# Kernel optimization log

Measured on AMD Instinct MI355X. Metric: run time of the kernel, lower is better.

## Reference

```python
import jax, jax.numpy as jnp
import numpy as np

T, B, H, L = 512, 64, 512, 2  # seq_len, batch, hidden(=input), num_layers


def setup_inputs() -> dict:
    key = jax.random.key(0)
    ks = jax.random.split(key, 15)
    s = 1.0 / np.sqrt(H)
    u = lambda k, shape: jax.random.uniform(k, shape, jnp.float32, -s, s)
    return {
        "sequence_r": jax.random.normal(ks[0], (T, B, H), jnp.float32),
        "sequence_i": jax.random.normal(ks[1], (T, B, H), jnp.float32),
        "h0_r": jax.random.normal(ks[2], (L, B, H), jnp.float32),
        "h0_i": jax.random.normal(ks[3], (L, B, H), jnp.float32),
        "c0_r": jax.random.normal(ks[4], (L, B, H), jnp.float32),
        "c0_i": jax.random.normal(ks[5], (L, B, H), jnp.float32),
        # complexLinear weights: real and imag parts of input->4H and hidden->4H maps
        "Wi_r": u(ks[6], (L, 4 * H, H)),
        "Wi_i": u(ks[7], (L, 4 * H, H)),
        "Wh_r": u(ks[8], (L, 4 * H, H)),
        "Wh_i": u(ks[9], (L, 4 * H, H)),
        "bi_r": u(ks[10], (L, 4 * H)),
        "bi_i": u(ks[11], (L, 4 * H)),
        "bh_r": u(ks[12], (L, 4 * H)),
        "bh_i": u(ks[13], (L, 4 * H)),
    }


def _run_layer(xr, xi, hr, hi, cr, ci, wir, wii, whr, whi, bir, bii, bhr, bhi):
    # Precompute the input projection for all timesteps (complex matmul): [T,B,4H]
    pr = jnp.einsum('tbd,gd->tbg', xr, wir) - jnp.einsum('tbd,gd->tbg', xi, wii) + bir
    pi = jnp.einsum('tbd,gd->tbg', xi, wir) + jnp.einsum('tbd,gd->tbg', xr, wii) + bii

    def step(carry, p):
        hr, hi, cr, ci = carry
        prt, pit = p
        # complex hidden projection
        gr = prt + hr @ whr.T - hi @ whi.T + bhr  # [B,4H]
        gi = pit + hi @ whr.T + hr @ whi.T + bhi
        ir_, fr_, gr_, or_ = jnp.split(gr, 4, axis=-1)
        ii_, fi_, gi_, oi_ = jnp.split(gi, 4, axis=-1)
        # split-type complex activations: act(real) + 1j*act(imag)
        i_r, i_i = jax.nn.sigmoid(ir_), jax.nn.sigmoid(ii_)
        f_r, f_i = jax.nn.sigmoid(fr_), jax.nn.sigmoid(fi_)
        o_r, o_i = jax.nn.sigmoid(or_), jax.nn.sigmoid(oi_)
        g_r, g_i = jnp.tanh(gr_), jnp.tanh(gi_)
        # c = f*c + i*g  (complex multiply)
        cr2 = f_r * cr - f_i * ci + i_r * g_r - i_i * g_i
        ci2 = f_r * ci + f_i * cr + i_r * g_i + i_i * g_r
        # h = o * tanh(c)
        t_r, t_i = jnp.tanh(cr2), jnp.tanh(ci2)
        hr2 = o_r * t_r - o_i * t_i
        hi2 = o_r * t_i + o_i * t_r
        return (hr2, hi2, cr2, ci2), (hr2, hi2)

    (hr, hi, cr, ci), (yr, yi) = jax.lax.scan(step, (hr, hi, cr, ci), (pr, pi))
    return yr, yi, hr, hi


def reference(sequence_r, sequence_i, h0_r, h0_i, c0_r, c0_i,
              Wi_r, Wi_i, Wh_r, Wh_i, bi_r, bi_i, bh_r, bh_i):
    xr, xi = sequence_r, sequence_i
    fin_r, fin_i = [], []
    for l in range(h0_r.shape[0]):
        xr, xi, hr, hi = _run_layer(
            xr, xi, h0_r[l], h0_i[l], c0_r[l], c0_i[l],
            Wi_r[l], Wi_i[l], Wh_r[l], Wh_i[l],
            bi_r[l], bi_i[l], bh_r[l], bh_i[l])
        fin_r.append(hr)
        fin_i.append(hi)
    return xr, xi, jnp.stack(fin_r), jnp.stack(fin_i)
```

## Files before the change

### kernel.cpp

```cpp
#include <hip/hip_runtime.h>
#include <stdint.h>


#define NPHASE 514

typedef __attribute__((ext_vector_type(8))) short short8;
typedef __attribute__((ext_vector_type(4))) float floatx4;
typedef float __attribute__((ext_vector_type(4))) floatv4;
typedef __attribute__((ext_vector_type(4))) unsigned int uintx4;

#define OFF_W    32768u
#define SZ_W     (2u*4096u*2048u*2u)
#define OFF_BIAS (OFF_W + SZ_W)
#define SZ_BIAS  (2u*4096u*4u)
#define OFF_H    (OFF_BIAS + SZ_BIAS)
#define SZ_H     (2u*4u*64u*512u*4u)
#define OFF_XBF  (OFF_H + SZ_H)
#define SZ_XBF   (512u*64u*1024u*2u)
#define NEED_XBF ((size_t)OFF_XBF + SZ_XBF)

__device__ __forceinline__ unsigned short f2bf(float f) {
  union { float f; uint32_t u; } v; v.f = f;
  uint32_t u = v.u;
  uint32_t r = (u + 0x7fffu + ((u >> 16) & 1u)) >> 16;
  return (unsigned short)r;
}
__device__ __forceinline__ float sigm(float x)  { return 1.0f / (1.0f + __expf(-x)); }
__device__ __forceinline__ float tanhf_(float x){ return 1.0f - 2.0f / (1.0f + __expf(2.0f * x)); }

__device__ __forceinline__ uintx4 ld_bypass_b128(const uint32_t* p) {
  uintx4 r;
  asm volatile("global_load_dwordx4 %0, %1, off sc0 sc1" : "=v"(r) : "v"(p));
  return r;
}
__device__ __forceinline__ void wait_vm0() {
  asm volatile("s_waitcnt vmcnt(0)" ::: "memory");
  __builtin_amdgcn_sched_barrier(0);
}


__global__ void pack_weights_k(const float* __restrict__ Wi_r, const float* __restrict__ Wi_i,
                               const float* __restrict__ Wh_r, const float* __restrict__ Wh_i,
                               unsigned short* __restrict__ wp) {
  uint32_t idx = blockIdx.x * 256u + threadIdx.x;
  int j    = idx & 7;
  int lane = (idx >> 3) & 63;
  int nt   = (idx >> 9) & 1;
  int kt   = (idx >> 10) & 63;
  int nb   = (idx >> 16) & 127;
  int l    = idx >> 23;
  int mrow = lane & 15, quad = lane >> 4;
  int n_col = nt * 16 + mrow;
  int dd = n_col >> 3, g = n_col & 7;
  int jrow = (g & 3) * 512 + nb * 4 + dd;
  int k = kt * 32 + quad * 8 + j;
  bool im = (g >= 4);
  size_t ro = ((size_t)l * 2048 + jrow) * 512;
  float v;
  if (k < 1024 && l == 0) {
    int seg = k >> 9, kk = k & 511;
    if (seg == 0) v = im ? Wi_i[ro + kk] :  Wi_r[ro + kk];
    else          v = im ? Wi_r[ro + kk] : -Wi_i[ro + kk];
  } else {
    int kk = k & 1023;
    int d = kk >> 1, ri = kk & 1;
    const float* Wr = (k < 1024) ? Wi_r : Wh_r;
    const float* Wm = (k < 1024) ? Wi_i : Wh_i;
    if (ri == 0) v = im ? Wm[ro + d] :  Wr[ro + d];
    else         v = im ? Wr[ro + d] : -Wm[ro + d];
  }
  wp[idx] = f2bf(v);
}

__global__ void pack_bias_k(const float* __restrict__ bi_r, const float* __restrict__ bi_i,
                            const float* __restrict__ bh_r, const float* __restrict__ bh_i,
                            float* __restrict__ bp) {
  uint32_t idx = blockIdx.x * 256u + threadIdx.x;
  int n_col = idx & 31, nb = (idx >> 5) & 127, l = idx >> 12;
  int dd = n_col >> 3, g = n_col & 7;
  int j = (g & 3) * 512 + nb * 4 + dd;
  float v = (g >= 4) ? (bi_i[l * 2048 + j] + bh_i[l * 2048 + j])
                     : (bi_r[l * 2048 + j] + bh_r[l * 2048 + j]);
  bp[idx] = v;
}

__global__ void init_state_k(const float* __restrict__ h0_r, const float* __restrict__ h0_i,
                             uint32_t* __restrict__ hring32, uint32_t* __restrict__ bar) {
  uint32_t idx = blockIdx.x * 256u + threadIdx.x;
  if (idx < 8192) bar[idx] = 0;
  int d = idx & 511, b = (idx >> 9) & 63, l = idx >> 15;
  int slot = (2 * l + 3) & 3;
  uint32_t* row = hring32 + (((size_t)l * 4 + slot) * 64 + b) * 512;
  row[d] = ((uint32_t)f2bf(h0_i[idx]) << 16) | (uint32_t)f2bf(h0_r[idx]);
}

__global__ void convert_x_k(const float* __restrict__ xr, const float* __restrict__ xi,
                            unsigned short* __restrict__ xbf) {
  uint32_t idx = blockIdx.x * 256u + threadIdx.x;
  int k = idx & 1023;
  uint32_t row = idx >> 10;
  float v = (k < 512) ? xr[(size_t)row * 512 + k] : xi[(size_t)row * 512 + (k - 512)];
  xbf[idx] = f2bf(v);
}


__global__ __launch_bounds__(256, 1) void lstm_persist_k(
    const float* __restrict__ xr, const float* __restrict__ xi,
    const float* __restrict__ c0_r, const float* __restrict__ c0_i,
    const unsigned short* __restrict__ wp, const float* __restrict__ bp,
    uint32_t* __restrict__ hring32, const unsigned short* __restrict__ xbf,
    float* __restrict__ out, uint32_t* arr, uint32_t* gen_bc, int use_xbf)
{
  __shared__ short8 Wb[8192];
  __shared__ float Glds[64 * 33];
  __shared__ float bias_s[32];

  const int l   = blockIdx.x >> 7;
  const int nb  = blockIdx.x & 127;
  const int bid = blockIdx.x;
  const int tid = threadIdx.x;

  {
    const short8* src = (const short8*)(wp + (((size_t)l * 128 + nb) << 16));
    #pragma unroll
    for (int i = 0; i < 32; ++i) Wb[i * 256 + tid] = src[i * 256 + tid];
    if (tid < 32) bias_s[tid] = bp[(l * 128 + nb) * 32 + tid];
  }

  const int b_e = tid & 63, dd_e = tid >> 6;
  const int d_e = nb * 4 + dd_e;
  float cr = c0_r[(l * 64 + b_e) * 512 + d_e];
  float ci = c0_i[(l * 64 + b_e) * 512 + d_e];
  __syncthreads();

  const int wv = tid >> 6, lane = tid & 63;
  const int quad = lane >> 4, mrow = lane & 15;
  const int bm = wv * 16 + mrow;
  const bool cvt_path = (l == 0) && (!use_xbf);

  for (int p = 0; p < NPHASE; ++p) {
    const int t = p - 2 * l;
    const bool active = (t >= 0) && (t < 512);
    floatx4 acc0 = {0.f, 0.f, 0.f, 0.f}, acc1 = {0.f, 0.f, 0.f, 0.f};

    if (active) {
      if (l == 0) {
        if (cvt_path) {
          const size_t xtb = ((size_t)t * 64 + bm) * 512 + quad * 8;
          #pragma unroll 8
          for (int kt = 0; kt < 32; ++kt) {
            const float* xb = ((kt < 16) ? xr : xi) + xtb + (kt & 15) * 32;
            floatv4 f0 = *(const floatv4*)xb;
            floatv4 f1 = *(const floatv4*)(xb + 4);
            short8 a;
            #pragma unroll
            for (int jj = 0; jj < 4; ++jj) { a[jj] = (short)f2bf(f0[jj]); a[jj+4] = (short)f2bf(f1[jj]); }
            short8 bf0 = Wb[(kt * 2 + 0) * 64 + lane];
            short8 bf1 = Wb[(kt * 2 + 1) * 64 + lane];
            acc0 = __builtin_amdgcn_mfma_f32_16x16x32_bf16(a, bf0, acc0, 0, 0, 0);
            acc1 = __builtin_amdgcn_mfma_f32_16x16x32_bf16(a, bf1, acc1, 0, 0, 0);
          }
        } else {
          const unsigned short* xb = xbf + ((size_t)t * 64 + bm) * 1024 + quad * 8;
          #pragma unroll 8
          for (int kt = 0; kt < 32; ++kt) {
            short8 a = *(const short8*)(xb + kt * 32);
            short8 bf0 = Wb[(kt * 2 + 0) * 64 + lane];
            short8 bf1 = Wb[(kt * 2 + 1) * 64 + lane];
            acc0 = __builtin_amdgcn_mfma_f32_16x16x32_bf16(a, bf0, acc0, 0, 0, 0);
            acc1 = __builtin_amdgcn_mfma_f32_16x16x32_bf16(a, bf1, acc1, 0, 0, 0);
          }
        }
      } else {
        const uint32_t* xb = hring32 + (((size_t)0 * 4 + ((p - 2) & 3)) * 64 + bm) * 512 + quad * 4;
        uintx4 xp[32];
        #pragma unroll
        for (int i = 0; i < 32; ++i) xp[i] = ld_bypass_b128(xb + i * 16);
        wait_vm0();
        #pragma unroll
        for (int i = 0; i < 32; ++i) {
          short8 a = __builtin_bit_cast(short8, xp[i]);
          short8 bf0 = Wb[(i * 2 + 0) * 64 + lane];
          short8 bf1 = Wb[(i * 2 + 1) * 64 + lane];
          acc0 = __builtin_amdgcn_mfma_f32_16x16x32_bf16(a, bf0, acc0, 0, 0, 0);
          acc1 = __builtin_amdgcn_mfma_f32_16x16x32_bf16(a, bf1, acc1, 0, 0, 0);
        }
      }
    }

    {
      const uint32_t g = (uint32_t)p;
      long budget = (1L << 22);
      if (bid == 0) {
        if (tid > 0) {
          while (__hip_atomic_load(&arr[tid * 16], __ATOMIC_RELAXED, __HIP_MEMORY_SCOPE_AGENT) < g) {
            if (--budget <= 0) break;
          }
        }
        __syncthreads();
        __hip_atomic_store(&gen_bc[tid * 16], g, __ATOMIC_RELAXED, __HIP_MEMORY_SCOPE_AGENT);
      } else {
        if (tid < 64) {
          while (__hip_atomic_load(&gen_bc[bid * 16], __ATOMIC_RELAXED, __HIP_MEMORY_SCOPE_AGENT) < g) {
            if (--budget <= 0) break;
          }
        }
        __syncthreads();
      }
    }

    if (active) {
      const uint32_t* hb = hring32 + (((size_t)l * 4 + ((p - 1) & 3)) * 64 + bm) * 512 + quad * 4;
      uintx4 hp[32];
      #pragma unroll
      for (int i = 0; i < 32; ++i) hp[i] = ld_bypass_b128(hb + i * 16);
      wait_vm0();
      #pragma unroll
      for (int i = 0; i < 32; ++i) {
        short8 a = __builtin_bit_cast(short8, hp[i]);
        short8 bf0 = Wb[((32 + i) * 2 + 0) * 64 + lane];
        short8 bf1 = Wb[((32 + i) * 2 + 1) * 64 + lane];
        acc0 = __builtin_amdgcn_mfma_f32_16x16x32_bf16(a, bf0, acc0, 0, 0, 0);
        acc1 = __builtin_amdgcn_mfma_f32_16x16x32_bf16(a, bf1, acc1, 0, 0, 0);
      }
      const float bb0 = bias_s[mrow], bb1 = bias_s[16 + mrow];
      const int rowb = wv * 16 + quad * 4;
      #pragma unroll
      for (int r = 0; r < 4; ++r) {
        Glds[(rowb + r) * 33 + mrow]      = acc0[r] + bb0;
        Glds[(rowb + r) * 33 + 16 + mrow] = acc1[r] + bb1;
      }
    }
    __syncthreads();
    if (active) {
      const float* gp = &Glds[b_e * 33 + dd_e * 8];
      float i_r = sigm(gp[0]), f_r = sigm(gp[1]), gc_r = tanhf_(gp[2]), o_r = sigm(gp[3]);
      float i_i = sigm(gp[4]), f_i = sigm(gp[5]), gc_i = tanhf_(gp[6]), o_i = sigm(gp[7]);
      float cr2 = f_r * cr - f_i * ci + i_r * gc_r - i_i * gc_i;
      float ci2 = f_r * ci + f_i * cr + i_r * gc_i + i_i * gc_r;
      cr = cr2; ci = ci2;
      float t_r = tanhf_(cr), t_i = tanhf_(ci);
      float h_r = o_r * t_r - o_i * t_i;
      float h_i = o_r * t_i + o_i * t_r;
      uint32_t hpk = ((uint32_t)f2bf(h_i) << 16) | (uint32_t)f2bf(h_r);
      uint32_t* hw = hring32 + (((size_t)l * 4 + (p & 3)) * 64 + b_e) * 512;
      __hip_atomic_store(&hw[d_e], hpk, __ATOMIC_RELAXED, __HIP_MEMORY_SCOPE_AGENT);
      if (l == 1) {
        size_t o = ((size_t)t * 64 + b_e) * 512 + d_e;
        __hip_atomic_store((uint32_t*)(out + o), __float_as_uint(h_r),
                           __ATOMIC_RELAXED, __HIP_MEMORY_SCOPE_AGENT);
        __hip_atomic_store((uint32_t*)(out + 16777216 + o), __float_as_uint(h_i),
                           __ATOMIC_RELAXED, __HIP_MEMORY_SCOPE_AGENT);
      }
      if (t == 511) {
        size_t o = 33554432u + ((size_t)l * 64 + b_e) * 512 + d_e;
        __hip_atomic_store((uint32_t*)(out + o), __float_as_uint(h_r),
                           __ATOMIC_RELAXED, __HIP_MEMORY_SCOPE_AGENT);
        __hip_atomic_store((uint32_t*)(out + o + 65536), __float_as_uint(h_i),
                           __ATOMIC_RELAXED, __HIP_MEMORY_SCOPE_AGENT);
      }
    }
    __syncthreads();
    if (bid != 0 && tid == 0)
      __hip_atomic_store(&arr[bid * 16], (uint32_t)(p + 1),
                         __ATOMIC_RELAXED, __HIP_MEMORY_SCOPE_AGENT);
  }
}


extern "C" void kernel_launch(void* const* d_in, const int* in_sizes, int n_in,
                              void* d_out, int out_size, void* d_ws, size_t ws_size,
                              hipStream_t stream) {
  const float* seq_r = (const float*)d_in[0];
  const float* seq_i = (const float*)d_in[1];
  const float* h0_r  = (const float*)d_in[2];
  const float* h0_i  = (const float*)d_in[3];
  const float* c0_r  = (const float*)d_in[4];
  const float* c0_i  = (const float*)d_in[5];
  const float* Wi_r  = (const float*)d_in[6];
  const float* Wi_i  = (const float*)d_in[7];
  const float* Wh_r  = (const float*)d_in[8];
  const float* Wh_i  = (const float*)d_in[9];
  const float* bi_r  = (const float*)d_in[10];
  const float* bi_i  = (const float*)d_in[11];
  const float* bh_r  = (const float*)d_in[12];
  const float* bh_i  = (const float*)d_in[13];

  char* ws = (char*)d_ws;
  uint32_t* arr    = (uint32_t*)ws;
  uint32_t* gen_bc = (uint32_t*)(ws + 16384);
  unsigned short* wp   = (unsigned short*)(ws + OFF_W);
  float*          bias = (float*)(ws + OFF_BIAS);
  uint32_t*       hrg  = (uint32_t*)(ws + OFF_H);
  unsigned short* xbf  = (unsigned short*)(ws + OFF_XBF);
  const int use_xbf = (ws_size >= NEED_XBF) ? 1 : 0;

  pack_weights_k<<<65536, 256, 0, stream>>>(Wi_r, Wi_i, Wh_r, Wh_i, wp);
  pack_bias_k<<<32, 256, 0, stream>>>(bi_r, bi_i, bh_r, bh_i, bias);
  init_state_k<<<256, 256, 0, stream>>>(h0_r, h0_i, hrg, arr);
  if (use_xbf) convert_x_k<<<131072, 256, 0, stream>>>(seq_r, seq_i, xbf);

  lstm_persist_k<<<256, 256, 0, stream>>>(seq_r, seq_i, c0_r, c0_i, wp, bias,
                                          hrg, xbf, (float*)d_out, arr, gen_bc, use_xbf);
}
```

Before: 7.024 ms.

## Replace h ring buffer with full-history slots and coalesce h/output stores via LDS

Replaces the 4-slot hidden-state ring with a 513-slot history buffer per layer. Because each slot is written exactly once, readers can use ordinary cached loads with a pipelined unroll instead of cache-bypassing loads and a full vmcnt wait. It also stages each block's h values and outputs in LDS and writes them as 128-bit vector stores from single waves, rather than scalar atomic stores per thread. The history buffer needs much more workspace, and correctness now depends on cached loads never returning stale data for a slot written by another CU.

```diff
diff --git a/kernel.cpp b/kernel.cpp
--- a/kernel.cpp
+++ b/kernel.cpp
@@ -14,10 +14,11 @@
 #define OFF_BIAS (OFF_W + SZ_W)
 #define SZ_BIAS  (2u*4096u*4u)
 #define OFF_H    (OFF_BIAS + SZ_BIAS)
-#define SZ_H     (2u*4u*64u*512u*4u)
+#define SZ_H     (2u*513u*64u*512u*4u)
 #define OFF_XBF  (OFF_H + SZ_H)
 #define SZ_XBF   (512u*64u*1024u*2u)
-#define NEED_XBF ((size_t)OFF_XBF + SZ_XBF)
+#define NEED_HIST ((size_t)OFF_XBF)
+#define NEED_XBF  ((size_t)OFF_XBF + SZ_XBF)
 
 __device__ __forceinline__ unsigned short f2bf(float f) {
   union { float f; uint32_t u; } v; v.f = f;
@@ -32,6 +33,9 @@
   uintx4 r;
   asm volatile("global_load_dwordx4 %0, %1, off sc0 sc1" : "=v"(r) : "v"(p));
   return r;
+}
+__device__ __forceinline__ void st_thru_b128(uint32_t* p, uintx4 v) {
+  asm volatile("global_store_dwordx4 %0, %1, off sc0 sc1" :: "v"(p), "v"(v) : "memory");
 }
 __device__ __forceinline__ void wait_vm0() {
   asm volatile("s_waitcnt vmcnt(0)" ::: "memory");
@@ -85,12 +89,13 @@
 }
 
 __global__ void init_state_k(const float* __restrict__ h0_r, const float* __restrict__ h0_i,
-                             uint32_t* __restrict__ hring32, uint32_t* __restrict__ bar) {
+                             uint32_t* __restrict__ hist, uint32_t* __restrict__ bar,
+                             int use_hist) {
   uint32_t idx = blockIdx.x * 256u + threadIdx.x;
   if (idx < 8192) bar[idx] = 0;
   int d = idx & 511, b = (idx >> 9) & 63, l = idx >> 15;
-  int slot = (2 * l + 3) & 3;
-  uint32_t* row = hring32 + (((size_t)l * 4 + slot) * 64 + b) * 512;
+  size_t NS = use_hist ? 513 : 4;
+  uint32_t* row = hist + ((size_t)l * NS + 0) * 32768 + (size_t)b * 512;
   row[d] = ((uint32_t)f2bf(h0_i[idx]) << 16) | (uint32_t)f2bf(h0_r[idx]);
 }
 
@@ -108,12 +113,15 @@
     const float* __restrict__ xr, const float* __restrict__ xi,
     const float* __restrict__ c0_r, const float* __restrict__ c0_i,
     const unsigned short* __restrict__ wp, const float* __restrict__ bp,
-    uint32_t* __restrict__ hring32, const unsigned short* __restrict__ xbf,
-    float* __restrict__ out, uint32_t* arr, uint32_t* gen_bc, int use_xbf)
+    uint32_t* __restrict__ hist, const unsigned short* __restrict__ xbf,
+    float* __restrict__ out, uint32_t* arr, uint32_t* gen_bc,
+    int use_xbf, int use_hist)
 {
   __shared__ short8 Wb[8192];
   __shared__ float Glds[64 * 33];
   __shared__ float bias_s[32];
+  __shared__ uint32_t hbuf[64 * 4];
+  __shared__ float obr[64 * 4], obi[64 * 4];
 
   const int l   = blockIdx.x >> 7;
   const int nb  = blockIdx.x & 127;
@@ -137,6 +145,11 @@
   const int quad = lane >> 4, mrow = lane & 15;
   const int bm = wv * 16 + mrow;
   const bool cvt_path = (l == 0) && (!use_xbf);
+
+  const size_t NS = use_hist ? 513 : 4;
+  uint32_t* hbase_l = hist + (size_t)l * NS * 32768;
+  uint32_t* hbase_0 = hist;
+  auto sidx = [&](int s) -> size_t { return use_hist ? (size_t)s : (size_t)(s & 3); };
 
   for (int p = 0; p < NPHASE; ++p) {
     const int t = p - 2 * l;
@@ -172,18 +185,29 @@
           }
         }
       } else {
-        const uint32_t* xb = hring32 + (((size_t)0 * 4 + ((p - 2) & 3)) * 64 + bm) * 512 + quad * 4;
-        uintx4 xp[32];
-        #pragma unroll
-        for (int i = 0; i < 32; ++i) xp[i] = ld_bypass_b128(xb + i * 16);
-        wait_vm0();
-        #pragma unroll
-        for (int i = 0; i < 32; ++i) {
-          short8 a = __builtin_bit_cast(short8, xp[i]);
-          short8 bf0 = Wb[(i * 2 + 0) * 64 + lane];
-          short8 bf1 = Wb[(i * 2 + 1) * 64 + lane];
-          acc0 = __builtin_amdgcn_mfma_f32_16x16x32_bf16(a, bf0, acc0, 0, 0, 0);
-          acc1 = __builtin_amdgcn_mfma_f32_16x16x32_bf16(a, bf1, acc1, 0, 0, 0);
+        const uint32_t* xb = hbase_0 + sidx(p - 1) * 32768 + (size_t)bm * 512 + quad * 4;
+        if (use_hist) {
+          #pragma unroll 8
+          for (int i = 0; i < 32; ++i) {
+            short8 a = __builtin_bit_cast(short8, *(const uintx4*)(xb + i * 16));
+            short8 bf0 = Wb[(i * 2 + 0) * 64 + lane];
+            short8 bf1 = Wb[(i * 2 + 1) * 64 + lane];
+            acc0 = __builtin_amdgcn_mfma_f32_16x16x32_bf16(a, bf0, acc0, 0, 0, 0);
+            acc1 = __builtin_amdgcn_mfma_f32_16x16x32_bf16(a, bf1, acc1, 0, 0, 0);
+          }
+        } else {
+          uintx4 xp[32];
+          #pragma unroll
+          for (int i = 0; i < 32; ++i) xp[i] = ld_bypass_b128(xb + i * 16);
+          wait_vm0();
+          #pragma unroll
+          for (int i = 0; i < 32; ++i) {
+            short8 a = __builtin_bit_cast(short8, xp[i]);
+            short8 bf0 = Wb[(i * 2 + 0) * 64 + lane];
+            short8 bf1 = Wb[(i * 2 + 1) * 64 + lane];
+            acc0 = __builtin_amdgcn_mfma_f32_16x16x32_bf16(a, bf0, acc0, 0, 0, 0);
+            acc1 = __builtin_amdgcn_mfma_f32_16x16x32_bf16(a, bf1, acc1, 0, 0, 0);
+          }
         }
       }
     }
@@ -210,18 +234,29 @@
     }
 
     if (active) {
-      const uint32_t* hb = hring32 + (((size_t)l * 4 + ((p - 1) & 3)) * 64 + bm) * 512 + quad * 4;
-      uintx4 hp[32];
-      #pragma unroll
-      for (int i = 0; i < 32; ++i) hp[i] = ld_bypass_b128(hb + i * 16);
-      wait_vm0();
-      #pragma unroll
-      for (int i = 0; i < 32; ++i) {
-        short8 a = __builtin_bit_cast(short8, hp[i]);
-        short8 bf0 = Wb[((32 + i) * 2 + 0) * 64 + lane];
-        short8 bf1 = Wb[((32 + i) * 2 + 1) * 64 + lane];
-        acc0 = __builtin_amdgcn_mfma_f32_16x16x32_bf16(a, bf0, acc0, 0, 0, 0);
-        acc1 = __builtin_amdgcn_mfma_f32_16x16x32_bf16(a, bf1, acc1, 0, 0, 0);
+      const uint32_t* hb = hbase_l + sidx(t) * 32768 + (size_t)bm * 512 + quad * 4;
+      if (use_hist) {
+        #pragma unroll 8
+        for (int i = 0; i < 32; ++i) {
+          short8 a = __builtin_bit_cast(short8, *(const uintx4*)(hb + i * 16));
+          short8 bf0 = Wb[((32 + i) * 2 + 0) * 64 + lane];
+          short8 bf1 = Wb[((32 + i) * 2 + 1) * 64 + lane];
+          acc0 = __builtin_amdgcn_mfma_f32_16x16x32_bf16(a, bf0, acc0, 0, 0, 0);
+          acc1 = __builtin_amdgcn_mfma_f32_16x16x32_bf16(a, bf1, acc1, 0, 0, 0);
+        }
+      } else {
+        uintx4 hp[32];
+        #pragma unroll
+        for (int i = 0; i < 32; ++i) hp[i] = ld_bypass_b128(hb + i * 16);
+        wait_vm0();
+        #pragma unroll
+        for (int i = 0; i < 32; ++i) {
+          short8 a = __builtin_bit_cast(short8, hp[i]);
+          short8 bf0 = Wb[((32 + i) * 2 + 0) * 64 + lane];
+          short8 bf1 = Wb[((32 + i) * 2 + 1) * 64 + lane];
+          acc0 = __builtin_amdgcn_mfma_f32_16x16x32_bf16(a, bf0, acc0, 0, 0, 0);
+          acc1 = __builtin_amdgcn_mfma_f32_16x16x32_bf16(a, bf1, acc1, 0, 0, 0);
+        }
       }
       const float bb0 = bias_s[mrow], bb1 = bias_s[16 + mrow];
       const int rowb = wv * 16 + quad * 4;
@@ -232,6 +267,7 @@
       }
     }
     __syncthreads();
+
     if (active) {
       const float* gp = &Glds[b_e * 33 + dd_e * 8];
       float i_r = sigm(gp[0]), f_r = sigm(gp[1]), gc_r = tanhf_(gp[2]), o_r = sigm(gp[3]);
@@ -242,28 +278,35 @@
       float t_r = tanhf_(cr), t_i = tanhf_(ci);
       float h_r = o_r * t_r - o_i * t_i;
       float h_i = o_r * t_i + o_i * t_r;
-      uint32_t hpk = ((uint32_t)f2bf(h_i) << 16) | (uint32_t)f2bf(h_r);
-      uint32_t* hw = hring32 + (((size_t)l * 4 + (p & 3)) * 64 + b_e) * 512;
-      __hip_atomic_store(&hw[d_e], hpk, __ATOMIC_RELAXED, __HIP_MEMORY_SCOPE_AGENT);
-      if (l == 1) {
-        size_t o = ((size_t)t * 64 + b_e) * 512 + d_e;
-        __hip_atomic_store((uint32_t*)(out + o), __float_as_uint(h_r),
+      hbuf[b_e * 4 + dd_e] = ((uint32_t)f2bf(h_i) << 16) | (uint32_t)f2bf(h_r);
+      obr[b_e * 4 + dd_e] = h_r;
+      obi[b_e * 4 + dd_e] = h_i;
+    }
+    __syncthreads();
+
+    if (active) {
+      if (wv == 0) {
+        uintx4 hv = *(const uintx4*)&hbuf[lane * 4];
+        st_thru_b128(hbase_l + sidx(t + 1) * 32768 + (size_t)lane * 512 + nb * 4, hv);
+      } else if (l == 1 && wv == 1) {
+        floatv4 ov = *(const floatv4*)&obr[lane * 4];
+        *(floatv4*)(out + ((size_t)t * 64 + lane) * 512 + nb * 4) = ov;
+      } else if (l == 1 && wv == 2) {
+        floatv4 ov = *(const floatv4*)&obi[lane * 4];
+        *(floatv4*)(out + 16777216u + ((size_t)t * 64 + lane) * 512 + nb * 4) = ov;
+      }
+      if (t == 511 && wv == 3) {
+        size_t o = 33554432u + ((size_t)l * 64 + lane) * 512 + nb * 4;
+        *(floatv4*)(out + o)         = *(const floatv4*)&obr[lane * 4];
+        *(floatv4*)(out + o + 65536) = *(const floatv4*)&obi[lane * 4];
+      }
+    }
+    if (wv == 0) {
+      asm volatile("s_waitcnt vmcnt(0)" ::: "memory");
+      if (bid != 0 && tid == 0)
+        __hip_atomic_store(&arr[bid * 16], (uint32_t)(p + 1),
                            __ATOMIC_RELAXED, __HIP_MEMORY_SCOPE_AGENT);
-        __hip_atomic_store((uint32_t*)(out + 16777216 + o), __float_as_uint(h_i),
-                           __ATOMIC_RELAXED, __HIP_MEMORY_SCOPE_AGENT);
-      }
-      if (t == 511) {
-        size_t o = 33554432u + ((size_t)l * 64 + b_e) * 512 + d_e;
-        __hip_atomic_store((uint32_t*)(out + o), __float_as_uint(h_r),
-                           __ATOMIC_RELAXED, __HIP_MEMORY_SCOPE_AGENT);
-        __hip_atomic_store((uint32_t*)(out + o + 65536), __float_as_uint(h_i),
-                           __ATOMIC_RELAXED, __HIP_MEMORY_SCOPE_AGENT);
-      }
-    }
-    __syncthreads();
-    if (bid != 0 && tid == 0)
-      __hip_atomic_store(&arr[bid * 16], (uint32_t)(p + 1),
-                         __ATOMIC_RELAXED, __HIP_MEMORY_SCOPE_AGENT);
+    }
   }
 }
 
@@ -291,15 +334,17 @@
   uint32_t* gen_bc = (uint32_t*)(ws + 16384);
   unsigned short* wp   = (unsigned short*)(ws + OFF_W);
   float*          bias = (float*)(ws + OFF_BIAS);
-  uint32_t*       hrg  = (uint32_t*)(ws + OFF_H);
+  uint32_t*       hist = (uint32_t*)(ws + OFF_H);
   unsigned short* xbf  = (unsigned short*)(ws + OFF_XBF);
-  const int use_xbf = (ws_size >= NEED_XBF) ? 1 : 0;
+  const int use_hist = (ws_size >= NEED_HIST) ? 1 : 0;
+  const int use_xbf  = (ws_size >= NEED_XBF) ? 1 : 0;
 
   pack_weights_k<<<65536, 256, 0, stream>>>(Wi_r, Wi_i, Wh_r, Wh_i, wp);
   pack_bias_k<<<32, 256, 0, stream>>>(bi_r, bi_i, bh_r, bh_i, bias);
-  init_state_k<<<256, 256, 0, stream>>>(h0_r, h0_i, hrg, arr);
+  init_state_k<<<256, 256, 0, stream>>>(h0_r, h0_i, hist, arr, use_hist);
   if (use_xbf) convert_x_k<<<131072, 256, 0, stream>>>(seq_r, seq_i, xbf);
 
   lstm_persist_k<<<256, 256, 0, stream>>>(seq_r, seq_i, c0_r, c0_i, wp, bias,
-                                          hrg, xbf, (float*)d_out, arr, gen_bc, use_xbf);
-}
+                                          hist, xbf, (float*)d_out, arr, gen_bc,
+                                          use_xbf, use_hist);
+}
```

After: 9.649 ms. 37.4% more time.

## Hold recurrent weights in registers, halve LDS weights, defer output stores past barrier

Applied to the files above, without the earlier changes.

Each lane now keeps the hidden-to-gate weight fragments (64 short8) in registers for the whole run instead of reading them from LDS every step, which halves the LDS weight buffer. The layer-1 input-h load is split into two halves of 16 loads to cut register pressure. The hidden ring indexing changes to be based on timestep, so layer 1 reads layer 0's newest slot one phase earlier. The output stores become plain stores issued after the arrival signal, taking them off the critical barrier path. The risk is heavy VGPR use (256 extra registers per lane) and possible spills.

```diff
diff --git a/kernel.cpp b/kernel.cpp
--- a/kernel.cpp
+++ b/kernel.cpp
@@ -89,8 +89,7 @@
   uint32_t idx = blockIdx.x * 256u + threadIdx.x;
   if (idx < 8192) bar[idx] = 0;
   int d = idx & 511, b = (idx >> 9) & 63, l = idx >> 15;
-  int slot = (2 * l + 3) & 3;
-  uint32_t* row = hring32 + (((size_t)l * 4 + slot) * 64 + b) * 512;
+  uint32_t* row = hring32 + ((size_t)l * 4) * 32768 + (size_t)b * 512;
   row[d] = ((uint32_t)f2bf(h0_i[idx]) << 16) | (uint32_t)f2bf(h0_r[idx]);
 }
 
@@ -111,7 +110,7 @@
     uint32_t* __restrict__ hring32, const unsigned short* __restrict__ xbf,
     float* __restrict__ out, uint32_t* arr, uint32_t* gen_bc, int use_xbf)
 {
-  __shared__ short8 Wb[8192];
+  __shared__ short8 Wb[4096];
   __shared__ float Glds[64 * 33];
   __shared__ float bias_s[32];
 
@@ -119,12 +118,22 @@
   const int nb  = blockIdx.x & 127;
   const int bid = blockIdx.x;
   const int tid = threadIdx.x;
+  const int wv = tid >> 6, lane = tid & 63;
+  const int quad = lane >> 4, mrow = lane & 15;
+  const int bm = wv * 16 + mrow;
 
   {
     const short8* src = (const short8*)(wp + (((size_t)l * 128 + nb) << 16));
     #pragma unroll
-    for (int i = 0; i < 32; ++i) Wb[i * 256 + tid] = src[i * 256 + tid];
+    for (int i = 0; i < 16; ++i) Wb[i * 256 + tid] = src[i * 256 + tid];
     if (tid < 32) bias_s[tid] = bp[(l * 128 + nb) * 32 + tid];
+  }
+
+  short8 wh[64];
+  {
+    const short8* wsrc = (const short8*)wp + ((size_t)(l * 128 + nb) * 8192);
+    #pragma unroll
+    for (int m = 0; m < 64; ++m) wh[m] = wsrc[(64 + m) * 64 + lane];
   }
 
   const int b_e = tid & 63, dd_e = tid >> 6;
@@ -133,10 +142,8 @@
   float ci = c0_i[(l * 64 + b_e) * 512 + d_e];
   __syncthreads();
 
-  const int wv = tid >> 6, lane = tid & 63;
-  const int quad = lane >> 4, mrow = lane & 15;
-  const int bm = wv * 16 + mrow;
   const bool cvt_path = (l == 0) && (!use_xbf);
+  uint32_t* hbase_l = hring32 + (size_t)l * 4 * 32768;
 
   for (int p = 0; p < NPHASE; ++p) {
     const int t = p - 2 * l;
@@ -172,18 +179,22 @@
           }
         }
       } else {
-        const uint32_t* xb = hring32 + (((size_t)0 * 4 + ((p - 2) & 3)) * 64 + bm) * 512 + quad * 4;
-        uintx4 xp[32];
+        const uint32_t* xb = hring32 + ((size_t)((p - 1) & 3) * 64 + bm) * 512 + quad * 4;
         #pragma unroll
-        for (int i = 0; i < 32; ++i) xp[i] = ld_bypass_b128(xb + i * 16);
-        wait_vm0();
-        #pragma unroll
-        for (int i = 0; i < 32; ++i) {
-          short8 a = __builtin_bit_cast(short8, xp[i]);
-          short8 bf0 = Wb[(i * 2 + 0) * 64 + lane];
-          short8 bf1 = Wb[(i * 2 + 1) * 64 + lane];
-          acc0 = __builtin_amdgcn_mfma_f32_16x16x32_bf16(a, bf0, acc0, 0, 0, 0);
-          acc1 = __builtin_amdgcn_mfma_f32_16x16x32_bf16(a, bf1, acc1, 0, 0, 0);
+        for (int half = 0; half < 2; ++half) {
+          uintx4 xp[16];
+          #pragma unroll
+          for (int i = 0; i < 16; ++i) xp[i] = ld_bypass_b128(xb + (half * 16 + i) * 16);
+          wait_vm0();
+          #pragma unroll
+          for (int i = 0; i < 16; ++i) {
+            const int kt = half * 16 + i;
+            short8 a = __builtin_bit_cast(short8, xp[i]);
+            short8 bf0 = Wb[(kt * 2 + 0) * 64 + lane];
+            short8 bf1 = Wb[(kt * 2 + 1) * 64 + lane];
+            acc0 = __builtin_amdgcn_mfma_f32_16x16x32_bf16(a, bf0, acc0, 0, 0, 0);
+            acc1 = __builtin_amdgcn_mfma_f32_16x16x32_bf16(a, bf1, acc1, 0, 0, 0);
+          }
         }
       }
     }
@@ -210,7 +221,7 @@
     }
 
     if (active) {
-      const uint32_t* hb = hring32 + (((size_t)l * 4 + ((p - 1) & 3)) * 64 + bm) * 512 + quad * 4;
+      const uint32_t* hb = hbase_l + ((size_t)(t & 3) * 64 + bm) * 512 + quad * 4;
       uintx4 hp[32];
       #pragma unroll
       for (int i = 0; i < 32; ++i) hp[i] = ld_bypass_b128(hb + i * 16);
@@ -218,10 +229,8 @@
       #pragma unroll
       for (int i = 0; i < 32; ++i) {
         short8 a = __builtin_bit_cast(short8, hp[i]);
-        short8 bf0 = Wb[((32 + i) * 2 + 0) * 64 + lane];
-        short8 bf1 = Wb[((32 + i) * 2 + 1) * 64 + lane];
-        acc0 = __builtin_amdgcn_mfma_f32_16x16x32_bf16(a, bf0, acc0, 0, 0, 0);
-        acc1 = __builtin_amdgcn_mfma_f32_16x16x32_bf16(a, bf1, acc1, 0, 0, 0);
+        acc0 = __builtin_amdgcn_mfma_f32_16x16x32_bf16(a, wh[2 * i],     acc0, 0, 0, 0);
+        acc1 = __builtin_amdgcn_mfma_f32_16x16x32_bf16(a, wh[2 * i + 1], acc1, 0, 0, 0);
       }
       const float bb0 = bias_s[mrow], bb1 = bias_s[16 + mrow];
       const int rowb = wv * 16 + quad * 4;
@@ -232,6 +241,8 @@
       }
     }
     __syncthreads();
+
+    float h_r = 0.f, h_i = 0.f;
     if (active) {
       const float* gp = &Glds[b_e * 33 + dd_e * 8];
       float i_r = sigm(gp[0]), f_r = sigm(gp[1]), gc_r = tanhf_(gp[2]), o_r = sigm(gp[3]);
@@ -240,30 +251,29 @@
       float ci2 = f_r * ci + f_i * cr + i_r * gc_i + i_i * gc_r;
       cr = cr2; ci = ci2;
       float t_r = tanhf_(cr), t_i = tanhf_(ci);
-      float h_r = o_r * t_r - o_i * t_i;
-      float h_i = o_r * t_i + o_i * t_r;
+      h_r = o_r * t_r - o_i * t_i;
+      h_i = o_r * t_i + o_i * t_r;
       uint32_t hpk = ((uint32_t)f2bf(h_i) << 16) | (uint32_t)f2bf(h_r);
-      uint32_t* hw = hring32 + (((size_t)l * 4 + (p & 3)) * 64 + b_e) * 512;
-      __hip_atomic_store(&hw[d_e], hpk, __ATOMIC_RELAXED, __HIP_MEMORY_SCOPE_AGENT);
-      if (l == 1) {
-        size_t o = ((size_t)t * 64 + b_e) * 512 + d_e;
-        __hip_atomic_store((uint32_t*)(out + o), __float_as_uint(h_r),
-                           __ATOMIC_RELAXED, __HIP_MEMORY_SCOPE_AGENT);
-        __hip_atomic_store((uint32_t*)(out + 16777216 + o), __float_as_uint(h_i),
-                           __ATOMIC_RELAXED, __HIP_MEMORY_SCOPE_AGENT);
-      }
-      if (t == 511) {
-        size_t o = 33554432u + ((size_t)l * 64 + b_e) * 512 + d_e;
-        __hip_atomic_store((uint32_t*)(out + o), __float_as_uint(h_r),
-                           __ATOMIC_RELAXED, __HIP_MEMORY_SCOPE_AGENT);
-        __hip_atomic_store((uint32_t*)(out + o + 65536), __float_as_uint(h_i),
-                           __ATOMIC_RELAXED, __HIP_MEMORY_SCOPE_AGENT);
-      }
+      uint32_t* hw = hbase_l + ((size_t)((t + 1) & 3) * 64 + b_e) * 512 + d_e;
+      __hip_atomic_store(hw, hpk, __ATOMIC_RELAXED, __HIP_MEMORY_SCOPE_AGENT);
     }
     __syncthreads();
     if (bid != 0 && tid == 0)
       __hip_atomic_store(&arr[bid * 16], (uint32_t)(p + 1),
                          __ATOMIC_RELAXED, __HIP_MEMORY_SCOPE_AGENT);
+
+    if (active) {
+      if (l == 1) {
+        size_t o = ((size_t)t * 64 + b_e) * 512 + d_e;
+        out[o]             = h_r;
+        out[16777216u + o] = h_i;
+      }
+      if (t == 511) {
+        size_t o = 33554432u + ((size_t)l * 64 + b_e) * 512 + d_e;
+        out[o]          = h_r;
+        out[o + 65536u] = h_i;
+      }
+    }
   }
 }
 
```

Result: slower. 7.383 ms (+5.1%).

## Replace centralized grid barrier with all-to-all per-block flag matrix

Applied to the files above, without the earlier changes.

Replaces the two-level barrier (every block signals block 0, which then broadcasts a generation counter) with a 256x256 flag matrix. Each block writes its phase to every peer's row, and one wavefront polls its own row with 128-bit bypass loads. This removes the serialized gather-then-broadcast round trip from every timestep. It also remaps the element-wise threads so the four d values for a batch row sit in adjacent lanes, and moves the plain output stores after the flag publish. The cost is 256 flag stores per block per step plus a larger workspace region for the flags.

```diff
diff --git a/kernel.cpp b/kernel.cpp
--- a/kernel.cpp
+++ b/kernel.cpp
@@ -9,7 +9,7 @@
 typedef float __attribute__((ext_vector_type(4))) floatv4;
 typedef __attribute__((ext_vector_type(4))) unsigned int uintx4;
 
-#define OFF_W    32768u
+#define OFF_W    262144u
 #define SZ_W     (2u*4096u*2048u*2u)
 #define OFF_BIAS (OFF_W + SZ_W)
 #define SZ_BIAS  (2u*4096u*4u)
@@ -85,9 +85,9 @@
 }
 
 __global__ void init_state_k(const float* __restrict__ h0_r, const float* __restrict__ h0_i,
-                             uint32_t* __restrict__ hring32, uint32_t* __restrict__ bar) {
+                             uint32_t* __restrict__ hring32, uint32_t* __restrict__ flags) {
   uint32_t idx = blockIdx.x * 256u + threadIdx.x;
-  if (idx < 8192) bar[idx] = 0;
+  flags[idx] = 0;
   int d = idx & 511, b = (idx >> 9) & 63, l = idx >> 15;
   int slot = (2 * l + 3) & 3;
   uint32_t* row = hring32 + (((size_t)l * 4 + slot) * 64 + b) * 512;
@@ -109,7 +109,7 @@
     const float* __restrict__ c0_r, const float* __restrict__ c0_i,
     const unsigned short* __restrict__ wp, const float* __restrict__ bp,
     uint32_t* __restrict__ hring32, const unsigned short* __restrict__ xbf,
-    float* __restrict__ out, uint32_t* arr, uint32_t* gen_bc, int use_xbf)
+    float* __restrict__ out, uint32_t* flags, int use_xbf)
 {
   __shared__ short8 Wb[8192];
   __shared__ float Glds[64 * 33];
@@ -127,7 +127,7 @@
     if (tid < 32) bias_s[tid] = bp[(l * 128 + nb) * 32 + tid];
   }
 
-  const int b_e = tid & 63, dd_e = tid >> 6;
+  const int b_e = tid >> 2, dd_e = tid & 3;
   const int d_e = nb * 4 + dd_e;
   float cr = c0_r[(l * 64 + b_e) * 512 + d_e];
   float ci = c0_i[(l * 64 + b_e) * 512 + d_e];
@@ -190,23 +190,18 @@
 
     {
       const uint32_t g = (uint32_t)p;
-      long budget = (1L << 22);
-      if (bid == 0) {
-        if (tid > 0) {
-          while (__hip_atomic_load(&arr[tid * 16], __ATOMIC_RELAXED, __HIP_MEMORY_SCOPE_AGENT) < g) {
-            if (--budget <= 0) break;
-          }
+      if (wv == 0) {
+        const uint32_t* fp = flags + (size_t)bid * 256 + lane * 4;
+        long budget = (1L << 22);
+        for (;;) {
+          uintx4 v = ld_bypass_b128(fp);
+          wait_vm0();
+          bool ok = (v.x >= g) & (v.y >= g) & (v.z >= g) & (v.w >= g);
+          if (__all(ok)) break;
+          if (--budget <= 0) break;
         }
-        __syncthreads();
-        __hip_atomic_store(&gen_bc[tid * 16], g, __ATOMIC_RELAXED, __HIP_MEMORY_SCOPE_AGENT);
-      } else {
-        if (tid < 64) {
-          while (__hip_atomic_load(&gen_bc[bid * 16], __ATOMIC_RELAXED, __HIP_MEMORY_SCOPE_AGENT) < g) {
-            if (--budget <= 0) break;
-          }
-        }
-        __syncthreads();
-      }
+      }
+      __syncthreads();
     }
 
     if (active) {
@@ -232,6 +227,8 @@
       }
     }
     __syncthreads();
+
+    float h_r = 0.f, h_i = 0.f;
     if (active) {
       const float* gp = &Glds[b_e * 33 + dd_e * 8];
       float i_r = sigm(gp[0]), f_r = sigm(gp[1]), gc_r = tanhf_(gp[2]), o_r = sigm(gp[3]);
@@ -240,30 +237,29 @@
       float ci2 = f_r * ci + f_i * cr + i_r * gc_i + i_i * gc_r;
       cr = cr2; ci = ci2;
       float t_r = tanhf_(cr), t_i = tanhf_(ci);
-      float h_r = o_r * t_r - o_i * t_i;
-      float h_i = o_r * t_i + o_i * t_r;
+      h_r = o_r * t_r - o_i * t_i;
+      h_i = o_r * t_i + o_i * t_r;
       uint32_t hpk = ((uint32_t)f2bf(h_i) << 16) | (uint32_t)f2bf(h_r);
-      uint32_t* hw = hring32 + (((size_t)l * 4 + (p & 3)) * 64 + b_e) * 512;
-      __hip_atomic_store(&hw[d_e], hpk, __ATOMIC_RELAXED, __HIP_MEMORY_SCOPE_AGENT);
+      uint32_t* hw = hring32 + (((size_t)l * 4 + (p & 3)) * 64 + b_e) * 512 + d_e;
+      __hip_atomic_store(hw, hpk, __ATOMIC_RELAXED, __HIP_MEMORY_SCOPE_AGENT);
+    }
+    __syncthreads();
+
+    __hip_atomic_store(&flags[(size_t)tid * 256 + bid], (uint32_t)(p + 1),
+                       __ATOMIC_RELAXED, __HIP_MEMORY_SCOPE_AGENT);
+
+    if (active) {
       if (l == 1) {
         size_t o = ((size_t)t * 64 + b_e) * 512 + d_e;
-        __hip_atomic_store((uint32_t*)(out + o), __float_as_uint(h_r),
-                           __ATOMIC_RELAXED, __HIP_MEMORY_SCOPE_AGENT);
-        __hip_atomic_store((uint32_t*)(out + 16777216 + o), __float_as_uint(h_i),
-                           __ATOMIC_RELAXED, __HIP_MEMORY_SCOPE_AGENT);
+        out[o]             = h_r;
+        out[16777216u + o] = h_i;
       }
       if (t == 511) {
         size_t o = 33554432u + ((size_t)l * 64 + b_e) * 512 + d_e;
-        __hip_atomic_store((uint32_t*)(out + o), __float_as_uint(h_r),
-                           __ATOMIC_RELAXED, __HIP_MEMORY_SCOPE_AGENT);
-        __hip_atomic_store((uint32_t*)(out + o + 65536), __float_as_uint(h_i),
-                           __ATOMIC_RELAXED, __HIP_MEMORY_SCOPE_AGENT);
-      }
-    }
-    __syncthreads();
-    if (bid != 0 && tid == 0)
-      __hip_atomic_store(&arr[bid * 16], (uint32_t)(p + 1),
-                         __ATOMIC_RELAXED, __HIP_MEMORY_SCOPE_AGENT);
+        out[o]          = h_r;
+        out[o + 65536u] = h_i;
+      }
+    }
   }
 }
 
@@ -287,8 +283,7 @@
   const float* bh_i  = (const float*)d_in[13];
 
   char* ws = (char*)d_ws;
-  uint32_t* arr    = (uint32_t*)ws;
-  uint32_t* gen_bc = (uint32_t*)(ws + 16384);
+  uint32_t* flags  = (uint32_t*)ws;
   unsigned short* wp   = (unsigned short*)(ws + OFF_W);
   float*          bias = (float*)(ws + OFF_BIAS);
   uint32_t*       hrg  = (uint32_t*)(ws + OFF_H);
@@ -297,9 +292,9 @@
 
   pack_weights_k<<<65536, 256, 0, stream>>>(Wi_r, Wi_i, Wh_r, Wh_i, wp);
   pack_bias_k<<<32, 256, 0, stream>>>(bi_r, bi_i, bh_r, bh_i, bias);
-  init_state_k<<<256, 256, 0, stream>>>(h0_r, h0_i, hrg, arr);
+  init_state_k<<<256, 256, 0, stream>>>(h0_r, h0_i, hrg, flags);
   if (use_xbf) convert_x_k<<<131072, 256, 0, stream>>>(seq_r, seq_i, xbf);
 
   lstm_persist_k<<<256, 256, 0, stream>>>(seq_r, seq_i, c0_r, c0_i, wp, bias,
-                                          hrg, xbf, (float*)d_out, arr, gen_bc, use_xbf);
-}
+                                          hrg, xbf, (float*)d_out, flags, use_xbf);
+}
```

Result: faster. 6.537 ms (-6.9%).
